# Optimization experiments

Measured on AMD Instinct MI355X. Metric: run time of the kernel, lower is better.

Reference implementation:

```python
import jax, jax.numpy as jnp
import numpy as np

N_CLASSES = 43
N_PRIM_CAPS = 8
PRIM_DIM = 16  # out channels per primary capsule conv
N_NODES = 16 * 9 * 9  # 1296
OUT_DIM = 16
N_ITER = 3
DN = ('NCHW', 'OIHW', 'NCHW')


def squash(v):
    # scale = |v|^2/(1+|v|^2); out = scale * v / |v|
    sn = jnp.sum(v * v, axis=-1, keepdims=True)
    return (sn / (1.0 + sn)) * v / jnp.sqrt(sn)


def setup_inputs() -> dict:
    key = jax.random.key(0)
    ks = jax.random.split(key, 6)
    x = jax.random.normal(ks[0], (64, 3, 32, 32), dtype=jnp.float32)
    conv1_w = 0.05 * jax.random.normal(ks[1], (256, 3, 9, 9), dtype=jnp.float32)
    conv1_b = 0.05 * jax.random.normal(ks[2], (256,), dtype=jnp.float32)
    # 8 independent Conv2d(256,16,8,stride=2) stacked capsule-major into one conv
    prim_w = 0.05 * jax.random.normal(ks[3], (N_PRIM_CAPS * PRIM_DIM, 256, 8, 8), dtype=jnp.float32)
    prim_b = 0.05 * jax.random.normal(ks[4], (N_PRIM_CAPS * PRIM_DIM,), dtype=jnp.float32)
    # route_weights: (1, n_nodes, n_caps, in_C=8, out_C=16); leading 1 dropped
    route_w = 0.1 * jax.random.normal(ks[5], (N_NODES, N_CLASSES, N_PRIM_CAPS, OUT_DIM), dtype=jnp.float32)
    return {"x": x, "conv1_w": conv1_w, "conv1_b": conv1_b,
            "prim_w": prim_w, "prim_b": prim_b, "route_w": route_w}


def reference(x, conv1_w, conv1_b, prim_w, prim_b, route_w):
    B = x.shape[0]
    # conv1 + relu: [B,3,32,32] -> [B,256,24,24]
    h = jax.lax.conv_general_dilated(x, conv1_w, (1, 1), 'VALID', dimension_numbers=DN)
    h = jax.nn.relu(h + conv1_b[None, :, None, None])
    # primary capsules: 8 convs fused -> [B,128,9,9]
    p = jax.lax.conv_general_dilated(h, prim_w, (2, 2), 'VALID', dimension_numbers=DN)
    p = p + prim_b[None, :, None, None]
    # per-capsule flatten (16*9*9=1296) then stack capsules on last axis -> [B,1296,8]
    p = p.reshape(B, N_PRIM_CAPS, N_NODES).transpose(0, 2, 1)
    u = squash(p)
    # priors: [B, n_nodes, n_classes, out_dim]
    priors = jnp.einsum('bni,ncio->bnco', u, route_w)
    logits = jnp.zeros_like(priors)
    outputs = None
    for i in range(N_ITER):
        probs = jax.nn.softmax(logits, axis=2)  # softmax over class axis
        outputs = squash(jnp.sum(probs * priors, axis=1, keepdims=True))  # [B,1,C,16]
        if i != N_ITER - 1:
            delta = jnp.sum(priors * outputs, axis=-1, keepdims=True)  # [B,n,C,1]
            logits = logits + delta  # broadcasts to [B,n,C,16]
    v = outputs[:, 0]  # [B,43,16]
    scores = jnp.sqrt(jnp.sum(v * v, axis=-1))  # [B,43]
    return scores
```

## Files before the change

kernel.cpp:

```cpp
#include <hip/hip_runtime.h>
#include <hip/hip_bf16.h>
#include <math.h>

static constexpr size_t W1T_OFF  = 0;
static constexpr size_t W2T_OFF  = 62208;
static constexpr size_t H_OFF    = 1110784;
static constexpr size_t PPART_OFF= 5829376;
static constexpr size_t UT_OFF   = 11137792;
static constexpr size_t S0_OFF   = 11801344;
static constexpr size_t OUT0_OFF = 11845376;
static constexpr size_t S1_OFF   = 11889408;
static constexpr size_t OUT1_OFF = 11933440;
static constexpr size_t S2_OFF   = 11977472;
static constexpr size_t PKW_OFF  = 0;
static constexpr size_t L_OFF    = 3698688;
static constexpr size_t PR_OFF   = 7265280;

typedef __bf16 bf16x8 __attribute__((ext_vector_type(8)));
typedef float  f32x4  __attribute__((ext_vector_type(4)));

__device__ inline unsigned pk2(float a, float b) {
    __hip_bfloat162 h = __float22bfloat162_rn(make_float2(a, b));
    return *(unsigned*)&h;
}

__global__ void k_init(float* ws) {
    int g = blockIdx.x * 256 + threadIdx.x;
    ws[S0_OFF + g] = 0.f;
}

__global__ void k_packb1(float* ws, const float* w1) {
    int g = blockIdx.x * 256 + threadIdx.x;
    int lane = g & 63;
    int r = g >> 6;
    int nt = r & 3, s = (r >> 2) % 14, ocq = r / 56;
    int quad = lane >> 4;
    int oc = ocq * 64 + nt * 16 + (lane & 15);
    int grp = 2 * s + (quad >> 1);
    int kxb = (quad & 1) * 8;
    uint4 o = {0u, 0u, 0u, 0u};
    if (grp < 27) {
        const float* wp = w1 + (size_t)oc * 243 + grp * 9;
        float v[8];
#pragma unroll
        for (int j = 0; j < 8; ++j) {
            int kx = kxb + j;
            v[j] = (kx < 9) ? wp[kx] : 0.f;
        }
        o.x = pk2(v[0], v[1]); o.y = pk2(v[2], v[3]);
        o.z = pk2(v[4], v[5]); o.w = pk2(v[6], v[7]);
    }
    ((uint4*)(ws + W1T_OFF))[g] = o;
}

__global__ void k_pack2(float* ws, const float* w2) {
    int g = blockIdx.x * 256 + threadIdx.x;
    int s = g >> 9;
    int r = g & 511;
    int nt = r >> 6, lane = r & 63;
    int n = nt * 16 + (lane & 15);
    int k0 = s * 32 + (lane >> 4) * 8;
    const float4* src = (const float4*)(w2 + (size_t)n * 16384 + k0);
    float4 v0 = src[0], v1 = src[1];
    uint4 o;
    o.x = pk2(v0.x, v0.y); o.y = pk2(v0.z, v0.w);
    o.z = pk2(v1.x, v1.y); o.w = pk2(v1.z, v1.w);
    ((uint4*)(ws + W2T_OFF))[g] = o;
}

__global__ void k_packw(float* ws, const float* rw) {
    int g = blockIdx.x * 256 + threadIdx.x;
    int lane = g & 63;
    int e = g >> 6;
    int c = e / 336;
    int r = e % 336;
    int tile = r / 21, ks = r % 21;
    int quad = lane >> 4, o = lane & 15;
    int nl = ks * 4 + quad;
    uint4 out = {0u, 0u, 0u, 0u};
    if (nl < 81) {
        int n = tile * 81 + nl;
        const float* wp = rw + ((size_t)n * 43 + c) * 128 + o;
        out.x = pk2(wp[0],  wp[16]);
        out.y = pk2(wp[32], wp[48]);
        out.z = pk2(wp[64], wp[80]);
        out.w = pk2(wp[96], wp[112]);
    }
    ((uint4*)(ws + PKW_OFF))[g] = out;
}

__global__ __launch_bounds__(256, 1) void k_conv1_mfma(float* ws, const float* x,
                                                       const float* b1) {
    __shared__ float xf[3136];
    __shared__ unsigned xd[2][1552];
    int blk = blockIdx.x;
    int b = blk >> 2, ocq = blk & 3;
    int t = threadIdx.x;

    const float4* xg = (const float4*)(x + (size_t)b * 3072);
    float4* xf4 = (float4*)xf;
#pragma unroll
    for (int i = t; i < 784; i += 256)
        xf4[i] = (i < 768) ? xg[i] : make_float4(0.f, 0.f, 0.f, 0.f);
    __syncthreads();
    for (int i = t; i < 1552; i += 256) {
        float a0 = xf[2 * i], a1 = xf[2 * i + 1], a2 = xf[2 * i + 2];
        xd[0][i] = pk2(a0, a1);
        xd[1][i] = pk2(a1, a2);
    }
    __syncthreads();

    int w = t >> 6, lane = t & 63;
    int quad = lane >> 4, mrow = lane & 15;

    f32x4 acc[9][4];
#pragma unroll
    for (int mt = 0; mt < 9; ++mt)
#pragma unroll
        for (int nt = 0; nt < 4; ++nt) acc[mt][nt] = (f32x4){0.f, 0.f, 0.f, 0.f};

    int exo[9];
#pragma unroll
    for (int mt = 0; mt < 9; ++mt) {
        int p = (w * 9 + mt) * 16 + mrow;
        exo[mt] = (p / 24) * 32 + (p % 24) + (quad & 1) * 8;
    }

    const uint4* pkb = (const uint4*)(ws + W1T_OFF) + (size_t)(ocq * 56) * 64;
    int gh = quad >> 1;

    for (int s = 0; s < 14; ++s) {
        int g = 2 * s + gh;
        int goff = (g < 27) ? (g / 9) * 1024 + (g % 9) * 32 : 0;
        uint4 bfr[4];
#pragma unroll
        for (int nt = 0; nt < 4; ++nt) bfr[nt] = pkb[(size_t)(s * 4 + nt) * 64 + lane];
        union { unsigned u[4]; bf16x8 v; } afr[9];
#pragma unroll
        for (int mt = 0; mt < 9; ++mt) {
            int e = goff + exo[mt];
            const unsigned* xp = &xd[e & 1][e >> 1];
            afr[mt].u[0] = xp[0]; afr[mt].u[1] = xp[1];
            afr[mt].u[2] = xp[2]; afr[mt].u[3] = xp[3];
        }
#pragma unroll
        for (int nt = 0; nt < 4; ++nt) {
            union { uint4 u; bf16x8 v; } bv; bv.u = bfr[nt];
#pragma unroll
            for (int mt = 0; mt < 9; ++mt)
                acc[mt][nt] = __builtin_amdgcn_mfma_f32_16x16x32_bf16(
                    afr[mt].v, bv.v, acc[mt][nt], 0, 0, 0);
        }
    }

    unsigned short* hb = (unsigned short*)(ws + H_OFF);
#pragma unroll
    for (int nt = 0; nt < 4; ++nt) {
        int oc = ocq * 64 + nt * 16 + mrow;
        float bias = b1[oc];
        unsigned* hp = (unsigned*)(hb + (size_t)(b * 256 + oc) * 576);
#pragma unroll
        for (int mt = 0; mt < 9; ++mt) {
            int p = (w * 9 + mt) * 16 + quad * 4;
            float v0 = fmaxf(acc[mt][nt][0] + bias, 0.f);
            float v1 = fmaxf(acc[mt][nt][1] + bias, 0.f);
            float v2 = fmaxf(acc[mt][nt][2] + bias, 0.f);
            float v3 = fmaxf(acc[mt][nt][3] + bias, 0.f);
            hp[(p >> 1) + 0] = pk2(v0, v1);
            hp[(p >> 1) + 1] = pk2(v2, v3);
        }
    }
}

__global__ __launch_bounds__(256, 4) void k_conv2_mfma(float* ws) {
    __shared__ unsigned short hs[2][2304];
    int blk = blockIdx.x;
    int b  = blk >> 4;
    int kq = (blk >> 1) & 7;
    int nh = blk & 1;
    int t = threadIdx.x;
    int w = t >> 6, lane = t & 63;
    int quad = lane >> 4, m = lane & 15;
    int mg = w >> 1, ng = w & 1;

    int aoy2[3], aox[3];
#pragma unroll
    for (int mi = 0; mi < 3; ++mi) {
        int p = (mg * 3 + mi) * 16 + m;
        if (p > 80) p = 0;
        aoy2[mi] = (p / 9) * 2;
        aox[mi] = p % 9;
    }

    const float4* hsg = (const float4*)((const unsigned short*)(ws + H_OFF)
                         + (size_t)(b * 256 + kq * 32) * 576);
    const uint4* wp = (const uint4*)(ws + W2T_OFF);
    int ntb = nh * 4 + ng * 2;

    f32x4 acc[3][2];
#pragma unroll
    for (int mi = 0; mi < 3; ++mi)
#pragma unroll
        for (int ni = 0; ni < 2; ++ni) acc[mi][ni] = (f32x4){0.f, 0.f, 0.f, 0.f};

    auto bidx = [&](int st, int cL, int ks, int ni) -> size_t {
        int s = (kq * 32 + st * 4 + cL) * 2 + ks;
        return (size_t)(s * 8 + ntb + ni) * 64 + lane;
    };

    ((float4*)&hs[0][0])[t] = hsg[t];
    if (t < 32) ((float4*)&hs[0][0])[256 + t] = hsg[256 + t];
    uint4 bc0 = wp[bidx(0, 0, 0, 0)], bc1 = wp[bidx(0, 0, 0, 1)];
    uint4 bc2 = wp[bidx(0, 0, 1, 0)], bc3 = wp[bidx(0, 0, 1, 1)];
    __syncthreads();

    for (int st = 0; st < 8; ++st) {
        float4 pre0, pre1;
        bool more = (st < 7);
        if (more) {
            pre0 = hsg[(st + 1) * 288 + t];
            if (t < 32) pre1 = hsg[(st + 1) * 288 + 256 + t];
        }
        const unsigned short* buf = &hs[st & 1][0];
#pragma unroll
        for (int cL = 0; cL < 4; ++cL) {
            int nst = (cL < 3) ? st : st + 1;
            int ncl = (cL < 3) ? cL + 1 : 0;
            bool pf = (nst < 8);
            uint4 bn0, bn1, bn2, bn3;
            if (pf) {
                bn0 = wp[bidx(nst, ncl, 0, 0)]; bn1 = wp[bidx(nst, ncl, 0, 1)];
                bn2 = wp[bidx(nst, ncl, 1, 0)]; bn3 = wp[bidx(nst, ncl, 1, 1)];
            }
            const unsigned short* cbuf = buf + cL * 576;
#pragma unroll
            for (int ks = 0; ks < 2; ++ks) {
                union { uint4 u; bf16x8 v; } bf0, bf1;
                bf0.u = ks ? bc2 : bc0;
                bf1.u = ks ? bc3 : bc1;
                int rowk = ks * 4 + quad;
#pragma unroll
                for (int mi = 0; mi < 3; ++mi) {
                    const unsigned int* ap =
                        (const unsigned int*)cbuf + (aoy2[mi] + rowk) * 12 + aox[mi];
                    union { unsigned int u[4]; bf16x8 v; } af;
                    af.u[0] = ap[0]; af.u[1] = ap[1]; af.u[2] = ap[2]; af.u[3] = ap[3];
                    acc[mi][0] = __builtin_amdgcn_mfma_f32_16x16x32_bf16(
                        af.v, bf0.v, acc[mi][0], 0, 0, 0);
                    acc[mi][1] = __builtin_amdgcn_mfma_f32_16x16x32_bf16(
                        af.v, bf1.v, acc[mi][1], 0, 0, 0);
                }
            }
            if (pf) { bc0 = bn0; bc1 = bn1; bc2 = bn2; bc3 = bn3; }
        }
        __syncthreads();
        if (more) {
            ((float4*)&hs[(st + 1) & 1][0])[t] = pre0;
            if (t < 32) ((float4*)&hs[(st + 1) & 1][0])[256 + t] = pre1;
        }
        __syncthreads();
    }

    float* pp = ws + PPART_OFF + ((size_t)(kq * 64 + b) * 81) * 128;
#pragma unroll
    for (int mi = 0; mi < 3; ++mi) {
#pragma unroll
        for (int ni = 0; ni < 2; ++ni) {
            int n = nh * 64 + (ng * 2 + ni) * 16 + m;
#pragma unroll
            for (int reg = 0; reg < 4; ++reg) {
                int p = (mg * 3 + mi) * 16 + quad * 4 + reg;
                if (p < 81) pp[(size_t)p * 128 + n] = acc[mi][ni][reg];
            }
        }
    }
}

__global__ void k_squash_u(float* ws, const float* prim_b) {
    __shared__ float vs[128];
    __shared__ float fac[16];
    int blk = blockIdx.x;
    int b = blk / 81, s = blk % 81;
    int n = threadIdx.x;
    const float* pp = ws + PPART_OFF;
    float v = prim_b[n];
#pragma unroll
    for (int kq = 0; kq < 8; ++kq)
        v += pp[((size_t)(kq * 64 + b) * 81 + s) * 128 + n];
    vs[n] = v;
    __syncthreads();
    if (n < 16) {
        float sn = 0.f;
#pragma unroll
        for (int i = 0; i < 8; ++i) { float tv = vs[i * 16 + n]; sn += tv * tv; }
        fac[n] = sqrtf(sn) / (1.f + sn);
    }
    __syncthreads();
    int i = n >> 4, d = n & 15;
    ws[UT_OFF + ((size_t)(d * 81 + s) * 64 + b) * 8 + i] = v * fac[d];
}

__global__ __launch_bounds__(256) void k_saccum_mfma(float* ws, const float* probs,
                                                     float* sdst) {
    int bx = blockIdx.x;
    int c = bx % 43, tile = bx / 43;
    int n0 = tile * 81;
    int t = threadIdx.x;
    int w = t >> 6, lane = t & 63;
    int quad = lane >> 4, m = lane & 15;
    int b = w * 16 + m;
    const float* ut = ws + UT_OFF;
    const uint4* pkw = (const uint4*)(ws + PKW_OFF)
                       + ((size_t)(c * 16 + tile) * 21) * 64 + lane;
    f32x4 acc = {0.f, 0.f, 0.f, 0.f};
#pragma unroll 7
    for (int ks = 0; ks < 21; ++ks) {
        int nl = ks * 4 + quad;
        union { uint4 u; bf16x8 v; } bf;
        bf.u = pkw[(size_t)ks * 64];
        union { unsigned u[4]; bf16x8 v; } af;
        af.u[0] = af.u[1] = af.u[2] = af.u[3] = 0u;
        if (nl < 81) {
            int n = n0 + nl;
            const float4* up = (const float4*)(ut + ((size_t)n * 64 + b) * 8);
            float4 u0 = up[0], u1 = up[1];
            float pv = probs ? probs[((size_t)n * 43 + c) * 64 + b] : 1.0f;
            af.u[0] = pk2(u0.x * pv, u0.y * pv);
            af.u[1] = pk2(u0.z * pv, u0.w * pv);
            af.u[2] = pk2(u1.x * pv, u1.y * pv);
            af.u[3] = pk2(u1.z * pv, u1.w * pv);
        }
        acc = __builtin_amdgcn_mfma_f32_16x16x32_bf16(af.v, bf.v, acc, 0, 0, 0);
    }
#pragma unroll
    for (int reg = 0; reg < 4; ++reg) {
        int bo = w * 16 + quad * 4 + reg;
        atomicAdd(sdst + ((size_t)bo * 43 + c) * 16 + m, acc[reg]);
    }
}

__global__ void k_outsquash(const float* s, float* ot, float scale) {
    int g = blockIdx.x * 256 + threadIdx.x;
    if (g >= 2752) return;
    int b = g / 43, c = g % 43;
    const float4* sp = (const float4*)(s + (size_t)g * 16);
    float v[16]; float sn = 0.f;
#pragma unroll
    for (int q = 0; q < 4; ++q) {
        float4 w = sp[q];
        v[q * 4] = w.x * scale; v[q * 4 + 1] = w.y * scale;
        v[q * 4 + 2] = w.z * scale; v[q * 4 + 3] = w.w * scale;
    }
#pragma unroll
    for (int j = 0; j < 16; ++j) sn += v[j] * v[j];
    float f = sqrtf(sn) / (1.f + sn);
    float4* op = (float4*)(ot + ((size_t)c * 64 + b) * 16);
#pragma unroll
    for (int q = 0; q < 4; ++q)
        op[q] = make_float4(v[q*4] * f, v[q*4+1] * f, v[q*4+2] * f, v[q*4+3] * f);
}

__global__ __launch_bounds__(256) void k_delta_mfma(float* ws, const float* outt,
                                                    float* L, int add) {
    int n = blockIdx.x, t = threadIdx.x;
    int w = t >> 6, lane = t & 63;
    int quad = lane >> 4, col = lane & 15;
    int b = w * 16 + col;

    union { unsigned u[4]; bf16x8 v; } bfrag;
    bfrag.u[0] = bfrag.u[1] = bfrag.u[2] = bfrag.u[3] = 0u;
    if (quad == 0) {
        const float4* up = (const float4*)(ws + UT_OFF + ((size_t)n * 64 + b) * 8);
        float4 u0 = up[0], u1 = up[1];
        bfrag.u[0] = pk2(u0.x, u0.y); bfrag.u[1] = pk2(u0.z, u0.w);
        bfrag.u[2] = pk2(u1.x, u1.y); bfrag.u[3] = pk2(u1.z, u1.w);
    }

    int tile = n / 81, nl = n % 81;
    int ks = nl >> 2, qpk = nl & 3;
    const uint4* pkw = (const uint4*)(ws + PKW_OFF);
    size_t abase = ((size_t)tile * 21 + ks) * 64 + qpk * 16 + col;
    const float4* ot4 = (const float4*)outt;
    size_t obase = (size_t)b * 4 + quad;

    uint4 a_cur = pkw[abase];
    float4 o_cur = ot4[obase];
    for (int c = 0; c < 43; ++c) {
        uint4 a_nxt; float4 o_nxt;
        if (c < 42) {
            a_nxt = pkw[abase + (size_t)(c + 1) * 21504];
            o_nxt = ot4[obase + (size_t)(c + 1) * 256];
        }
        union { uint4 u; bf16x8 v; } afrag; afrag.u = a_cur;
        f32x4 zero = {0.f, 0.f, 0.f, 0.f};
        f32x4 acc = __builtin_amdgcn_mfma_f32_16x16x32_bf16(afrag.v, bfrag.v, zero, 0, 0, 0);
        float val = acc[0] * o_cur.x + acc[1] * o_cur.y
                  + acc[2] * o_cur.z + acc[3] * o_cur.w;
        val += __shfl_xor(val, 16);
        val += __shfl_xor(val, 32);
        if (quad == 0) {
            size_t idx = ((size_t)n * 43 + c) * 64 + b;
            L[idx] = add ? (L[idx] + val) : val;
        }
        a_cur = a_nxt; o_cur = o_nxt;
    }
}

__global__ void k_softmax(const float* L, float* P) {
    int g = blockIdx.x * 256 + threadIdx.x;
    int n = g >> 6, b = g & 63;
    const float* lp = L + (size_t)n * 2752 + b;
    float v[43]; float m = -1e30f;
#pragma unroll
    for (int c = 0; c < 43; ++c) { v[c] = lp[c * 64]; m = fmaxf(m, v[c]); }
    float s = 0.f;
#pragma unroll
    for (int c = 0; c < 43; ++c) { v[c] = __expf(v[c] - m); s += v[c]; }
    float inv = 1.f / s;
    float* pp = P + (size_t)n * 2752 + b;
#pragma unroll
    for (int c = 0; c < 43; ++c) pp[c * 64] = v[c] * inv;
}

__global__ void k_scores(const float* s2, float* out) {
    int g = blockIdx.x * 256 + threadIdx.x;
    if (g >= 2752) return;
    const float4* sp = (const float4*)(s2 + (size_t)g * 16);
    float sn = 0.f;
#pragma unroll
    for (int q = 0; q < 4; ++q) {
        float4 w = sp[q];
        sn += w.x * w.x + w.y * w.y + w.z * w.z + w.w * w.w;
    }
    out[g] = sn / (1.f + sn);
}

extern "C" void kernel_launch(void* const* d_in, const int* in_sizes, int n_in,
                              void* d_out, int out_size, void* d_ws, size_t ws_size,
                              hipStream_t stream) {
    const float* x  = (const float*)d_in[0];
    const float* w1 = (const float*)d_in[1];
    const float* b1 = (const float*)d_in[2];
    const float* w2 = (const float*)d_in[3];
    const float* b2 = (const float*)d_in[4];
    const float* rw = (const float*)d_in[5];
    float* ws  = (float*)d_ws;
    float* out = (float*)d_out;

    k_init      <<<860,  256, 0, stream>>>(ws);
    k_packb1    <<<56,   256, 0, stream>>>(ws, w1);
    k_pack2     <<<1024, 256, 0, stream>>>(ws, w2);
    k_conv1_mfma<<<256,  256, 0, stream>>>(ws, x, b1);
    k_conv2_mfma<<<1024, 256, 0, stream>>>(ws);
    k_squash_u  <<<5184, 128, 0, stream>>>(ws, b2);
    k_packw     <<<3612, 256, 0, stream>>>(ws, rw);
    k_saccum_mfma<<<688, 256, 0, stream>>>(ws, nullptr, ws + S0_OFF);
    k_outsquash <<<11,  256, 0, stream>>>(ws + S0_OFF, ws + OUT0_OFF, 1.0f / 43.0f);
    k_delta_mfma<<<1296,256, 0, stream>>>(ws, ws + OUT0_OFF, ws + L_OFF, 0);
    k_softmax   <<<324, 256, 0, stream>>>(ws + L_OFF, ws + PR_OFF);
    k_saccum_mfma<<<688, 256, 0, stream>>>(ws, ws + PR_OFF, ws + S1_OFF);
    k_outsquash <<<11,  256, 0, stream>>>(ws + S1_OFF, ws + OUT1_OFF, 1.0f);
    k_delta_mfma<<<1296,256, 0, stream>>>(ws, ws + OUT1_OFF, ws + L_OFF, 1);
    k_softmax   <<<324, 256, 0, stream>>>(ws + L_OFF, ws + PR_OFF);
    k_saccum_mfma<<<688, 256, 0, stream>>>(ws, ws + PR_OFF, ws + S2_OFF);
    k_scores    <<<11,  256, 0, stream>>>(ws + S2_OFF, out);
}
```

Baseline: 268.3 us.

## Retile conv2 over batch pairs, merge pack kernels, replace atomics with partial sums

conv2 now has each block handle two batch images, with four N-tiles per wave, so every loaded weight fragment feeds twice as many MFMAs and the grid halves. The two weight-pack kernels become one launch. The capsule-sum accumulation writes per-tile partial sums instead of using atomicAdd, and the squash and score kernels reduce the 16 partials, which removes the zero-init kernel and atomic contention. In exchange, conv2 uses more registers and LDS per block, which lowers occupancy, and the reduction kernels read 16 times more data.

```diff
diff --git a/kernel.cpp b/kernel.cpp
--- a/kernel.cpp
+++ b/kernel.cpp
@@ -7,11 +7,9 @@
 static constexpr size_t H_OFF    = 1110784;
 static constexpr size_t PPART_OFF= 5829376;
 static constexpr size_t UT_OFF   = 11137792;
-static constexpr size_t S0_OFF   = 11801344;
-static constexpr size_t OUT0_OFF = 11845376;
-static constexpr size_t S1_OFF   = 11889408;
-static constexpr size_t OUT1_OFF = 11933440;
-static constexpr size_t S2_OFF   = 11977472;
+static constexpr size_t SPART_OFF= 11801344;
+static constexpr size_t OUT0_OFF = 12505856;
+static constexpr size_t OUT1_OFF = 12549888;
 static constexpr size_t PKW_OFF  = 0;
 static constexpr size_t L_OFF    = 3698688;
 static constexpr size_t PR_OFF   = 7265280;
@@ -24,48 +22,44 @@
     return *(unsigned*)&h;
 }
 
-__global__ void k_init(float* ws) {
-    int g = blockIdx.x * 256 + threadIdx.x;
-    ws[S0_OFF + g] = 0.f;
-}
-
-__global__ void k_packb1(float* ws, const float* w1) {
-    int g = blockIdx.x * 256 + threadIdx.x;
-    int lane = g & 63;
-    int r = g >> 6;
-    int nt = r & 3, s = (r >> 2) % 14, ocq = r / 56;
-    int quad = lane >> 4;
-    int oc = ocq * 64 + nt * 16 + (lane & 15);
-    int grp = 2 * s + (quad >> 1);
-    int kxb = (quad & 1) * 8;
-    uint4 o = {0u, 0u, 0u, 0u};
-    if (grp < 27) {
-        const float* wp = w1 + (size_t)oc * 243 + grp * 9;
-        float v[8];
-#pragma unroll
-        for (int j = 0; j < 8; ++j) {
-            int kx = kxb + j;
-            v[j] = (kx < 9) ? wp[kx] : 0.f;
-        }
-        o.x = pk2(v[0], v[1]); o.y = pk2(v[2], v[3]);
-        o.z = pk2(v[4], v[5]); o.w = pk2(v[6], v[7]);
-    }
-    ((uint4*)(ws + W1T_OFF))[g] = o;
-}
-
-__global__ void k_pack2(float* ws, const float* w2) {
-    int g = blockIdx.x * 256 + threadIdx.x;
-    int s = g >> 9;
-    int r = g & 511;
-    int nt = r >> 6, lane = r & 63;
-    int n = nt * 16 + (lane & 15);
-    int k0 = s * 32 + (lane >> 4) * 8;
-    const float4* src = (const float4*)(w2 + (size_t)n * 16384 + k0);
-    float4 v0 = src[0], v1 = src[1];
-    uint4 o;
-    o.x = pk2(v0.x, v0.y); o.y = pk2(v0.z, v0.w);
-    o.z = pk2(v1.x, v1.y); o.w = pk2(v1.z, v1.w);
-    ((uint4*)(ws + W2T_OFF))[g] = o;
+__global__ void k_packs(float* ws, const float* w1, const float* w2) {
+    int blk = blockIdx.x, t = threadIdx.x;
+    if (blk < 56) {
+        int g = blk * 256 + t;
+        int lane = g & 63;
+        int r = g >> 6;
+        int nt = r & 3, s = (r >> 2) % 14, ocq = r / 56;
+        int quad = lane >> 4;
+        int oc = ocq * 64 + nt * 16 + (lane & 15);
+        int grp = 2 * s + (quad >> 1);
+        int kxb = (quad & 1) * 8;
+        uint4 o = {0u, 0u, 0u, 0u};
+        if (grp < 27) {
+            const float* wp = w1 + (size_t)oc * 243 + grp * 9;
+            float v[8];
+#pragma unroll
+            for (int j = 0; j < 8; ++j) {
+                int kx = kxb + j;
+                v[j] = (kx < 9) ? wp[kx] : 0.f;
+            }
+            o.x = pk2(v[0], v[1]); o.y = pk2(v[2], v[3]);
+            o.z = pk2(v[4], v[5]); o.w = pk2(v[6], v[7]);
+        }
+        ((uint4*)(ws + W1T_OFF))[g] = o;
+    } else {
+        int g = (blk - 56) * 256 + t;
+        int s = g >> 9;
+        int r = g & 511;
+        int nt = r >> 6, lane = r & 63;
+        int n = nt * 16 + (lane & 15);
+        int k0 = s * 32 + (lane >> 4) * 8;
+        const float4* src = (const float4*)(w2 + (size_t)n * 16384 + k0);
+        float4 v0 = src[0], v1 = src[1];
+        uint4 o;
+        o.x = pk2(v0.x, v0.y); o.y = pk2(v0.z, v0.w);
+        o.z = pk2(v1.x, v1.y); o.w = pk2(v1.z, v1.w);
+        ((uint4*)(ws + W2T_OFF))[g] = o;
+    }
 }
 
 __global__ void k_packw(float* ws, const float* rw) {
@@ -172,16 +166,17 @@
     }
 }
 
-__global__ __launch_bounds__(256, 4) void k_conv2_mfma(float* ws) {
-    __shared__ unsigned short hs[2][2304];
+__global__ __launch_bounds__(256, 2) void k_conv2_mfma(float* ws) {
+    __shared__ unsigned short hs[2][4608];
     int blk = blockIdx.x;
-    int b  = blk >> 4;
+    int bp = blk >> 4;
     int kq = (blk >> 1) & 7;
     int nh = blk & 1;
+    int b0 = bp * 2;
     int t = threadIdx.x;
     int w = t >> 6, lane = t & 63;
     int quad = lane >> 4, m = lane & 15;
-    int mg = w >> 1, ng = w & 1;
+    int bw = w >> 1, mg = w & 1;
 
     int aoy2[3], aox[3];
 #pragma unroll
@@ -192,52 +187,63 @@
         aox[mi] = p % 9;
     }
 
-    const float4* hsg = (const float4*)((const unsigned short*)(ws + H_OFF)
-                         + (size_t)(b * 256 + kq * 32) * 576);
+    const unsigned short* hb = (const unsigned short*)(ws + H_OFF);
     const uint4* wp = (const uint4*)(ws + W2T_OFF);
-    int ntb = nh * 4 + ng * 2;
-
-    f32x4 acc[3][2];
+    int ntb = nh * 4;
+
+    f32x4 acc[3][4];
 #pragma unroll
     for (int mi = 0; mi < 3; ++mi)
 #pragma unroll
-        for (int ni = 0; ni < 2; ++ni) acc[mi][ni] = (f32x4){0.f, 0.f, 0.f, 0.f};
-
+        for (int ni = 0; ni < 4; ++ni) acc[mi][ni] = (f32x4){0.f, 0.f, 0.f, 0.f};
+
+    auto hsrc = [&](int st, int j) -> float4 {
+        int b2 = j / 288, r = j % 288;
+        int ch = r / 72, p4 = r % 72;
+        return ((const float4*)(hb + (size_t)((b0 + b2) * 256 + kq * 32 + st * 4 + ch) * 576))[p4];
+    };
     auto bidx = [&](int st, int cL, int ks, int ni) -> size_t {
         int s = (kq * 32 + st * 4 + cL) * 2 + ks;
         return (size_t)(s * 8 + ntb + ni) * 64 + lane;
     };
 
-    ((float4*)&hs[0][0])[t] = hsg[t];
-    if (t < 32) ((float4*)&hs[0][0])[256 + t] = hsg[256 + t];
-    uint4 bc0 = wp[bidx(0, 0, 0, 0)], bc1 = wp[bidx(0, 0, 0, 1)];
-    uint4 bc2 = wp[bidx(0, 0, 1, 0)], bc3 = wp[bidx(0, 0, 1, 1)];
+    {
+        float4* d = (float4*)&hs[0][0];
+        d[t] = hsrc(0, t);
+        d[256 + t] = hsrc(0, 256 + t);
+        if (t < 64) d[512 + t] = hsrc(0, 512 + t);
+    }
+    uint4 bc[2][4];
+#pragma unroll
+    for (int ks = 0; ks < 2; ++ks)
+#pragma unroll
+        for (int ni = 0; ni < 4; ++ni) bc[ks][ni] = wp[bidx(0, 0, ks, ni)];
     __syncthreads();
 
     for (int st = 0; st < 8; ++st) {
-        float4 pre0, pre1;
+        float4 pre0, pre1, pre2;
         bool more = (st < 7);
         if (more) {
-            pre0 = hsg[(st + 1) * 288 + t];
-            if (t < 32) pre1 = hsg[(st + 1) * 288 + 256 + t];
-        }
-        const unsigned short* buf = &hs[st & 1][0];
+            pre0 = hsrc(st + 1, t);
+            pre1 = hsrc(st + 1, 256 + t);
+            if (t < 64) pre2 = hsrc(st + 1, 512 + t);
+        }
+        const unsigned short* wbuf = &hs[st & 1][bw * 2304];
 #pragma unroll
         for (int cL = 0; cL < 4; ++cL) {
             int nst = (cL < 3) ? st : st + 1;
             int ncl = (cL < 3) ? cL + 1 : 0;
             bool pf = (nst < 8);
-            uint4 bn0, bn1, bn2, bn3;
+            uint4 bn[2][4];
             if (pf) {
-                bn0 = wp[bidx(nst, ncl, 0, 0)]; bn1 = wp[bidx(nst, ncl, 0, 1)];
-                bn2 = wp[bidx(nst, ncl, 1, 0)]; bn3 = wp[bidx(nst, ncl, 1, 1)];
+#pragma unroll
+                for (int ks = 0; ks < 2; ++ks)
+#pragma unroll
+                    for (int ni = 0; ni < 4; ++ni) bn[ks][ni] = wp[bidx(nst, ncl, ks, ni)];
             }
-            const unsigned short* cbuf = buf + cL * 576;
+            const unsigned short* cbuf = wbuf + cL * 576;
 #pragma unroll
             for (int ks = 0; ks < 2; ++ks) {
-                union { uint4 u; bf16x8 v; } bf0, bf1;
-                bf0.u = ks ? bc2 : bc0;
-                bf1.u = ks ? bc3 : bc1;
                 int rowk = ks * 4 + quad;
 #pragma unroll
                 for (int mi = 0; mi < 3; ++mi) {
@@ -245,28 +251,38 @@
                         (const unsigned int*)cbuf + (aoy2[mi] + rowk) * 12 + aox[mi];
                     union { unsigned int u[4]; bf16x8 v; } af;
                     af.u[0] = ap[0]; af.u[1] = ap[1]; af.u[2] = ap[2]; af.u[3] = ap[3];
-                    acc[mi][0] = __builtin_amdgcn_mfma_f32_16x16x32_bf16(
-                        af.v, bf0.v, acc[mi][0], 0, 0, 0);
-                    acc[mi][1] = __builtin_amdgcn_mfma_f32_16x16x32_bf16(
-                        af.v, bf1.v, acc[mi][1], 0, 0, 0);
+#pragma unroll
+                    for (int ni = 0; ni < 4; ++ni) {
+                        union { uint4 u; bf16x8 v; } bv; bv.u = bc[ks][ni];
+                        acc[mi][ni] = __builtin_amdgcn_mfma_f32_16x16x32_bf16(
+                            af.v, bv.v, acc[mi][ni], 0, 0, 0);
+                    }
                 }
             }
-            if (pf) { bc0 = bn0; bc1 = bn1; bc2 = bn2; bc3 = bn3; }
+            if (pf) {
+#pragma unroll
+                for (int ks = 0; ks < 2; ++ks)
+#pragma unroll
+                    for (int ni = 0; ni < 4; ++ni) bc[ks][ni] = bn[ks][ni];
+            }
         }
         __syncthreads();
         if (more) {
-            ((float4*)&hs[(st + 1) & 1][0])[t] = pre0;
-            if (t < 32) ((float4*)&hs[(st + 1) & 1][0])[256 + t] = pre1;
+            float4* d = (float4*)&hs[(st + 1) & 1][0];
+            d[t] = pre0;
+            d[256 + t] = pre1;
+            if (t < 64) d[512 + t] = pre2;
         }
         __syncthreads();
     }
 
+    int b = b0 + bw;
     float* pp = ws + PPART_OFF + ((size_t)(kq * 64 + b) * 81) * 128;
 #pragma unroll
     for (int mi = 0; mi < 3; ++mi) {
 #pragma unroll
-        for (int ni = 0; ni < 2; ++ni) {
-            int n = nh * 64 + (ng * 2 + ni) * 16 + m;
+        for (int ni = 0; ni < 4; ++ni) {
+            int n = (nh * 4 + ni) * 16 + m;
 #pragma unroll
             for (int reg = 0; reg < 4; ++reg) {
                 int p = (mg * 3 + mi) * 16 + quad * 4 + reg;
@@ -300,8 +316,7 @@
     ws[UT_OFF + ((size_t)(d * 81 + s) * 64 + b) * 8 + i] = v * fac[d];
 }
 
-__global__ __launch_bounds__(256) void k_saccum_mfma(float* ws, const float* probs,
-                                                     float* sdst) {
+__global__ __launch_bounds__(256) void k_saccum_mfma(float* ws, const float* probs) {
     int bx = blockIdx.x;
     int c = bx % 43, tile = bx / 43;
     int n0 = tile * 81;
@@ -332,24 +347,33 @@
         }
         acc = __builtin_amdgcn_mfma_f32_16x16x32_bf16(af.v, bf.v, acc, 0, 0, 0);
     }
+    float* sp = ws + SPART_OFF;
 #pragma unroll
     for (int reg = 0; reg < 4; ++reg) {
         int bo = w * 16 + quad * 4 + reg;
-        atomicAdd(sdst + ((size_t)bo * 43 + c) * 16 + m, acc[reg]);
-    }
-}
-
-__global__ void k_outsquash(const float* s, float* ot, float scale) {
+        sp[(((size_t)tile * 64 + bo) * 43 + c) * 16 + m] = acc[reg];
+    }
+}
+
+__global__ void k_outsquash(const float* spart, float* ot, float scale) {
     int g = blockIdx.x * 256 + threadIdx.x;
     if (g >= 2752) return;
     int b = g / 43, c = g % 43;
-    const float4* sp = (const float4*)(s + (size_t)g * 16);
+    float4 v4[4] = {{0,0,0,0},{0,0,0,0},{0,0,0,0},{0,0,0,0}};
+#pragma unroll
+    for (int tile = 0; tile < 16; ++tile) {
+        const float4* sp = (const float4*)(spart + (((size_t)tile * 64 + b) * 43 + c) * 16);
+#pragma unroll
+        for (int q = 0; q < 4; ++q) {
+            float4 wv = sp[q];
+            v4[q].x += wv.x; v4[q].y += wv.y; v4[q].z += wv.z; v4[q].w += wv.w;
+        }
+    }
     float v[16]; float sn = 0.f;
 #pragma unroll
     for (int q = 0; q < 4; ++q) {
-        float4 w = sp[q];
-        v[q * 4] = w.x * scale; v[q * 4 + 1] = w.y * scale;
-        v[q * 4 + 2] = w.z * scale; v[q * 4 + 3] = w.w * scale;
+        v[q * 4]     = v4[q].x * scale; v[q * 4 + 1] = v4[q].y * scale;
+        v[q * 4 + 2] = v4[q].z * scale; v[q * 4 + 3] = v4[q].w * scale;
     }
 #pragma unroll
     for (int j = 0; j < 16; ++j) sn += v[j] * v[j];
@@ -422,16 +446,24 @@
     for (int c = 0; c < 43; ++c) pp[c * 64] = v[c] * inv;
 }
 
-__global__ void k_scores(const float* s2, float* out) {
+__global__ void k_scores(const float* spart, float* out) {
     int g = blockIdx.x * 256 + threadIdx.x;
     if (g >= 2752) return;
-    const float4* sp = (const float4*)(s2 + (size_t)g * 16);
+    int b = g / 43, c = g % 43;
+    float4 v4[4] = {{0,0,0,0},{0,0,0,0},{0,0,0,0},{0,0,0,0}};
+#pragma unroll
+    for (int tile = 0; tile < 16; ++tile) {
+        const float4* sp = (const float4*)(spart + (((size_t)tile * 64 + b) * 43 + c) * 16);
+#pragma unroll
+        for (int q = 0; q < 4; ++q) {
+            float4 wv = sp[q];
+            v4[q].x += wv.x; v4[q].y += wv.y; v4[q].z += wv.z; v4[q].w += wv.w;
+        }
+    }
     float sn = 0.f;
 #pragma unroll
-    for (int q = 0; q < 4; ++q) {
-        float4 w = sp[q];
-        sn += w.x * w.x + w.y * w.y + w.z * w.z + w.w * w.w;
-    }
+    for (int q = 0; q < 4; ++q)
+        sn += v4[q].x * v4[q].x + v4[q].y * v4[q].y + v4[q].z * v4[q].z + v4[q].w * v4[q].w;
     out[g] = sn / (1.f + sn);
 }
 
@@ -447,21 +479,19 @@
     float* ws  = (float*)d_ws;
     float* out = (float*)d_out;
 
-    k_init      <<<860,  256, 0, stream>>>(ws);
-    k_packb1    <<<56,   256, 0, stream>>>(ws, w1);
-    k_pack2     <<<1024, 256, 0, stream>>>(ws, w2);
+    k_packs     <<<1080, 256, 0, stream>>>(ws, w1, w2);
     k_conv1_mfma<<<256,  256, 0, stream>>>(ws, x, b1);
-    k_conv2_mfma<<<1024, 256, 0, stream>>>(ws);
+    k_conv2_mfma<<<512,  256, 0, stream>>>(ws);
     k_squash_u  <<<5184, 128, 0, stream>>>(ws, b2);
     k_packw     <<<3612, 256, 0, stream>>>(ws, rw);
-    k_saccum_mfma<<<688, 256, 0, stream>>>(ws, nullptr, ws + S0_OFF);
-    k_outsquash <<<11,  256, 0, stream>>>(ws + S0_OFF, ws + OUT0_OFF, 1.0f / 43.0f);
+    k_saccum_mfma<<<688, 256, 0, stream>>>(ws, nullptr);
+    k_outsquash <<<11,  256, 0, stream>>>(ws + SPART_OFF, ws + OUT0_OFF, 1.0f / 43.0f);
     k_delta_mfma<<<1296,256, 0, stream>>>(ws, ws + OUT0_OFF, ws + L_OFF, 0);
     k_softmax   <<<324, 256, 0, stream>>>(ws + L_OFF, ws + PR_OFF);
-    k_saccum_mfma<<<688, 256, 0, stream>>>(ws, ws + PR_OFF, ws + S1_OFF);
-    k_outsquash <<<11,  256, 0, stream>>>(ws + S1_OFF, ws + OUT1_OFF, 1.0f);
+    k_saccum_mfma<<<688, 256, 0, stream>>>(ws, ws + PR_OFF);
+    k_outsquash <<<11,  256, 0, stream>>>(ws + SPART_OFF, ws + OUT1_OFF, 1.0f);
     k_delta_mfma<<<1296,256, 0, stream>>>(ws, ws + OUT1_OFF, ws + L_OFF, 1);
     k_softmax   <<<324, 256, 0, stream>>>(ws + L_OFF, ws + PR_OFF);
-    k_saccum_mfma<<<688, 256, 0, stream>>>(ws, ws + PR_OFF, ws + S2_OFF);
-    k_scores    <<<11,  256, 0, stream>>>(ws + S2_OFF, out);
-}
+    k_saccum_mfma<<<688, 256, 0, stream>>>(ws, ws + PR_OFF);
+    k_scores    <<<11,  256, 0, stream>>>(ws + SPART_OFF, out);
+}
```

New measurement: 281.7 us. 1.05x slower.
